# Performance work log

Measured on AMD Instinct MI355X. Metric: run time of the kernel, lower is better.

Reference implementation:

```python
import jax, jax.numpy as jnp
import numpy as np

# TT-factorized linear: 784 = 7*4*7*4 -> 512 = 4*4*8*4, max_rank=20
# canonical TT ranks: [1, 20, 20, 16, 1] (r3 capped by m4*n4 = 16)
B = 16384
R1, R2, R3 = 20, 20, 16


def setup_inputs() -> dict:
    key = jax.random.key(0)
    k = jax.random.split(key, 6)
    x = jax.random.normal(k[0], (B, 784), jnp.float32)
    # TT cores G_k[r_{k-1}, m_k, n_k, r_k] with boundary ranks squeezed
    core1 = jax.random.normal(k[1], (7, 4, R1), jnp.float32) * 0.3   # [m1,n1,r1]
    core2 = jax.random.normal(k[2], (R1, 4, 4, R2), jnp.float32) * 0.1  # [r1,m2,n2,r2]
    core3 = jax.random.normal(k[3], (R2, 7, 8, R3), jnp.float32) * 0.05  # [r2,m3,n3,r3]
    core4 = jax.random.normal(k[4], (R3, 4, 4), jnp.float32) * 0.1   # [r3,m4,n4]
    bias = jax.random.normal(k[5], (512,), jnp.float32) * 0.01
    return {"x": x, "core1": core1, "core2": core2, "core3": core3,
            "core4": core4, "bias": bias}


def reference(x, core1, core2, core3, core4, bias):
    b = x.shape[0]
    # reshape input into TT mode factorization [B, m1, m2, m3, m4]
    x5 = x.reshape(b, 7, 4, 7, 4)
    # chain of small core contractions (the fusion-opportunity op pattern)
    t = jnp.einsum('bijkl,ipr->bjklpr', x5, core1)   # [B,4,7,4, n1,r1]
    t = jnp.einsum('bjklpr,rjqs->bklpqs', t, core2)  # [B,7,4, n1,n2,r2]
    t = jnp.einsum('bklpqs,sket->blpqet', t, core3)  # [B,4, n1,n2,n3,r3]
    y = jnp.einsum('blpqet,tlf->bpqef', t, core4)    # [B, n1,n2,n3,n4]
    y = y.reshape(b, 512) + bias
    # original forward: relu then softmax over features.
    # NOTE: the source calls self.fc2(y) but discards the result, so it is
    # omitted here (no effect on output).
    return jax.nn.softmax(jax.nn.relu(y), axis=1)
```

## Files before the change

### kernel.cpp

```cpp
#include <hip/hip_runtime.h>


typedef __attribute__((ext_vector_type(8))) short short8;
typedef __attribute__((ext_vector_type(4))) float floatx4;

__device__ __forceinline__ unsigned int pack2_bf16(float a, float b) {
    unsigned int ua = __float_as_uint(a);
    unsigned int ub = __float_as_uint(b);
    return ((ub + 0x8000u) & 0xFFFF0000u) | ((ua + 0x8000u) >> 16);
}

__device__ __forceinline__ short f32_to_bf16_rne(float v) {
    unsigned int u = __float_as_uint(v);
    return (short)(((u + 0x7FFFu + ((u >> 16) & 1)) >> 16) & 0xFFFF);
}

__global__ void prep_all(const float* __restrict__ c1, const float* __restrict__ c2,
                         const float* __restrict__ c3, const float* __restrict__ c4,
                         short* __restrict__ wp) {
    const int tid = threadIdx.x;
    const int blk = blockIdx.x;
    if (blk == 224) {
        for (int e = tid; e < 8192; e += 256) {
            int j   = e & 7;
            int lid = (e >> 3) & 15;
            int q2  = (e >> 7) & 1;
            int tn  = e >> 8;
            wp[(((tn * 25 + 24) * 64 + (2 + q2) * 16 + lid) << 3) + j] = 0;
        }
        return;
    }
    __shared__ float t12s[320];
    __shared__ float t123s[7 * 256];
    __shared__ float c4s[256];

    const int ij    = blk >> 3;
    const int strip = blk & 7;
    const int i  = ij >> 2, j2 = ij & 3;
    const int p  = strip >> 1;
    const int qh = strip & 1;

    if (tid < 256) c4s[tid] = c4[tid];
    for (int e = tid; e < 320; e += 256) {
        int s = e % 20, pq = e / 20;
        int pp = pq >> 2, q = pq & 3;
        float acc = 0.f;
        #pragma unroll
        for (int r = 0; r < 20; ++r)
            acc += c1[i * 80 + pp * 20 + r] * c2[r * 320 + j2 * 80 + q * 20 + s];
        t12s[e] = acc;
    }
    __syncthreads();

    for (int e = tid; e < 1792; e += 256) {
        int k3 = e >> 8, li = e & 255;
        int t = li & 15, pql = li >> 4;
        int qloc = pql >> 3, e3 = pql & 7;
        int q = 2 * qh + qloc;
        float acc = 0.f;
        const float* tp = t12s + (p * 4 + q) * 20;
        const float* cp = c3 + k3 * 128 + e3 * 16 + t;
        #pragma unroll
        for (int s = 0; s < 20; ++s) acc += tp[s] * cp[s * 896];
        t123s[e] = acc;
    }
    __syncthreads();

    for (int e = tid; e < 1792; e += 256) {
        int kl = e >> 6, nl = e & 63;
        int k = ij * 28 + kl;
        int n = strip * 64 + nl;
        int k3 = kl >> 2, l = kl & 3;
        int f4 = n & 3, e3 = (n >> 2) & 7;
        int pql = ((n >> 5) & 1) * 8 + e3;
        const float* tp = t123s + k3 * 256 + pql * 16;
        const float* cq = c4s + l * 4 + f4;
        float a = 0.f;
        #pragma unroll
        for (int t = 0; t < 16; ++t) a += tp[t] * cq[t * 16];
        int tk = k >> 5, quad = (k >> 3) & 3, j = k & 7;
        int tn = n >> 4, lid = n & 15;
        wp[(((tn * 25 + tk) * 64 + quad * 16 + lid) << 3) + j] = f32_to_bf16_rne(a);
    }
}

__global__ __launch_bounds__(512, 4) void tt_gemm(const float* __restrict__ x,
                                                  const short* __restrict__ wp,
                                                  const float* __restrict__ bias,
                                                  float* __restrict__ out) {
    __shared__ __align__(16) short s_a[3200 * 8];
    __shared__ float part[8][32];

    const int tid  = threadIdx.x;
    const int w    = tid >> 6;
    const int lane = tid & 63;
    const int quad = lane >> 4;
    const int lid  = lane & 15;
    const int m_base = blockIdx.x * 32;

    const short* wpw = wp + ((size_t)(w * 4) * 25 * 64 + lane) * 8;

    short8 b_f[3][4];
    #pragma unroll
    for (int nt = 0; nt < 4; ++nt) {
        b_f[0][nt] = *(const short8*)(wpw + (size_t)(nt * 25 + 0) * 64 * 8);
        b_f[1][nt] = *(const short8*)(wpw + (size_t)(nt * 25 + 1) * 64 * 8);
    }

    for (int a = tid; a < 3200; a += 512) {
        const int row = ((a >> 6) & 1) * 16 + (a & 15);
        const int kc  = ((a >> 7) * 4 + ((a >> 4) & 3)) * 8;
        floatx4 v0 = {0.f, 0.f, 0.f, 0.f}, v1 = {0.f, 0.f, 0.f, 0.f};
        if (kc < 784) {
            const floatx4* pp = (const floatx4*)(x + (size_t)(m_base + row) * 784 + kc);
            v0 = pp[0]; v1 = pp[1];
        }
        union { short8 s; unsigned int u[4]; } af;
        af.u[0] = pack2_bf16(v0.x, v0.y);
        af.u[1] = pack2_bf16(v0.z, v0.w);
        af.u[2] = pack2_bf16(v1.x, v1.y);
        af.u[3] = pack2_bf16(v1.z, v1.w);
        *(short8*)&s_a[a * 8] = af.s;
    }
    __syncthreads();

    const short* sa = s_a + lane * 8;

    floatx4 acc[2][4];
    #pragma unroll
    for (int mt = 0; mt < 2; ++mt)
        #pragma unroll
        for (int nt = 0; nt < 4; ++nt)
            acc[mt][nt] = floatx4{0.f, 0.f, 0.f, 0.f};

    short8 a_f[2][2];
    a_f[0][0] = *(const short8*)(sa);
    a_f[0][1] = *(const short8*)(sa + 64 * 8);

    #pragma unroll
    for (int tk = 0; tk < 25; ++tk) {
        if (tk + 2 < 25) {
            #pragma unroll
            for (int nt = 0; nt < 4; ++nt)
                b_f[(tk + 2) % 3][nt] = *(const short8*)(wpw + (size_t)(nt * 25 + tk + 2) * 64 * 8);
        }
        if (tk + 1 < 25) {
            const short* sa2 = sa + (size_t)(tk + 1) * 128 * 8;
            a_f[(tk + 1) & 1][0] = *(const short8*)(sa2);
            a_f[(tk + 1) & 1][1] = *(const short8*)(sa2 + 64 * 8);
        }
        #pragma unroll
        for (int nt = 0; nt < 4; ++nt) {
            acc[0][nt] = __builtin_amdgcn_mfma_f32_16x16x32_bf16(a_f[tk & 1][0], b_f[tk % 3][nt], acc[0][nt], 0, 0, 0);
            acc[1][nt] = __builtin_amdgcn_mfma_f32_16x16x32_bf16(a_f[tk & 1][1], b_f[tk % 3][nt], acc[1][nt], 0, 0, 0);
        }
    }

    float bias_v[4];
    #pragma unroll
    for (int nt = 0; nt < 4; ++nt)
        bias_v[nt] = bias[w * 64 + nt * 16 + lid];

    #pragma unroll
    for (int mt = 0; mt < 2; ++mt) {
        #pragma unroll
        for (int reg = 0; reg < 4; ++reg) {
            float s = 0.f;
            #pragma unroll
            for (int nt = 0; nt < 4; ++nt) {
                float v = acc[mt][nt][reg] + bias_v[nt];
                v = fmaxf(v, 0.f);
                float e = __expf(v);
                acc[mt][nt][reg] = e;
                s += e;
            }
            s += __shfl_xor(s, 1, 64);
            s += __shfl_xor(s, 2, 64);
            s += __shfl_xor(s, 4, 64);
            s += __shfl_xor(s, 8, 64);
            if (lid == 0) part[w][mt * 16 + quad * 4 + reg] = s;
        }
    }
    __syncthreads();

    #pragma unroll
    for (int mt = 0; mt < 2; ++mt) {
        #pragma unroll
        for (int reg = 0; reg < 4; ++reg) {
            const int row = mt * 16 + quad * 4 + reg;
            float tot = 0.f;
            #pragma unroll
            for (int ww = 0; ww < 8; ++ww) tot += part[ww][row];
            const float inv = 1.0f / tot;
            #pragma unroll
            for (int nt = 0; nt < 4; ++nt)
                out[(size_t)(m_base + row) * 512 + w * 64 + nt * 16 + lid] = acc[mt][nt][reg] * inv;
        }
    }
}

extern "C" void kernel_launch(void* const* d_in, const int* in_sizes, int n_in,
                              void* d_out, int out_size, void* d_ws, size_t ws_size,
                              hipStream_t stream) {
    const float* x    = (const float*)d_in[0];
    const float* c1   = (const float*)d_in[1];
    const float* c2   = (const float*)d_in[2];
    const float* c3   = (const float*)d_in[3];
    const float* c4   = (const float*)d_in[4];
    const float* bias = (const float*)d_in[5];
    float* out = (float*)d_out;
    short* wpb = (short*)d_ws;

    prep_all<<<225, 256, 0, stream>>>(c1, c2, c3, c4, wpb);
    tt_gemm <<<512, 512, 0, stream>>>(x, wpb, bias, out);
}
```

Before: 125.7 us.

## Double-buffer A tile in LDS across five K-chunks to overlap loads with MFMA

Replaces the single full-K staging of the 32x784 activation tile in LDS with a two-buffer scheme over five K-chunks. Global loads for the next chunk are issued before the MFMA work on the current chunk, and are converted and written to LDS afterwards. B fragments are now loaded directly inside the loop rather than software-prefetched three deep. This shrinks LDS use (possibly raising occupancy) and hides global load latency behind compute, at the cost of extra barriers and less explicit B prefetching.

Result: no change. 126.5 us (+0.7%).

```diff
diff --git a/kernel.cpp b/kernel.cpp
--- a/kernel.cpp
+++ b/kernel.cpp
@@ -88,7 +88,7 @@
                                                   const short* __restrict__ wp,
                                                   const float* __restrict__ bias,
                                                   float* __restrict__ out) {
-    __shared__ __align__(16) short s_a[3200 * 8];
+    __shared__ __align__(16) short s_a[2][640 * 8];
     __shared__ float part[8][32];
 
     const int tid  = threadIdx.x;
@@ -97,34 +97,37 @@
     const int quad = lane >> 4;
     const int lid  = lane & 15;
     const int m_base = blockIdx.x * 32;
+    const bool two = (tid < 128);
 
     const short* wpw = wp + ((size_t)(w * 4) * 25 * 64 + lane) * 8;
 
-    short8 b_f[3][4];
-    #pragma unroll
-    for (int nt = 0; nt < 4; ++nt) {
-        b_f[0][nt] = *(const short8*)(wpw + (size_t)(nt * 25 + 0) * 64 * 8);
-        b_f[1][nt] = *(const short8*)(wpw + (size_t)(nt * 25 + 1) * 64 * 8);
-    }
-
-    for (int a = tid; a < 3200; a += 512) {
-        const int row = ((a >> 6) & 1) * 16 + (a & 15);
-        const int kc  = ((a >> 7) * 4 + ((a >> 4) & 3)) * 8;
-        floatx4 v0 = {0.f, 0.f, 0.f, 0.f}, v1 = {0.f, 0.f, 0.f, 0.f};
+    auto stage_load = [&](int c, int e, floatx4& v0, floatx4& v1) {
+        const int row = ((e >> 6) & 1) * 16 + (e & 15);
+        const int kc  = ((c * 5 + (e >> 7)) * 4 + ((e >> 4) & 3)) * 8;
+        v0 = floatx4{0.f, 0.f, 0.f, 0.f};
+        v1 = floatx4{0.f, 0.f, 0.f, 0.f};
         if (kc < 784) {
-            const floatx4* pp = (const floatx4*)(x + (size_t)(m_base + row) * 784 + kc);
-            v0 = pp[0]; v1 = pp[1];
-        }
+            const floatx4* p = (const floatx4*)(x + (size_t)(m_base + row) * 784 + kc);
+            v0 = p[0]; v1 = p[1];
+        }
+    };
+    auto stage_write = [&](int buf, int e, floatx4 v0, floatx4 v1) {
         union { short8 s; unsigned int u[4]; } af;
         af.u[0] = pack2_bf16(v0.x, v0.y);
         af.u[1] = pack2_bf16(v0.z, v0.w);
         af.u[2] = pack2_bf16(v1.x, v1.y);
         af.u[3] = pack2_bf16(v1.z, v1.w);
-        *(short8*)&s_a[a * 8] = af.s;
-    }
-    __syncthreads();
-
-    const short* sa = s_a + lane * 8;
+        *(short8*)&s_a[buf][e * 8] = af.s;
+    };
+
+    {
+        floatx4 a0, a1, b0, b1;
+        stage_load(0, tid, a0, a1);
+        if (two) stage_load(0, 512 + tid, b0, b1);
+        stage_write(0, tid, a0, a1);
+        if (two) stage_write(0, 512 + tid, b0, b1);
+    }
+    __syncthreads();
 
     floatx4 acc[2][4];
     #pragma unroll
@@ -133,26 +136,32 @@
         for (int nt = 0; nt < 4; ++nt)
             acc[mt][nt] = floatx4{0.f, 0.f, 0.f, 0.f};
 
-    short8 a_f[2][2];
-    a_f[0][0] = *(const short8*)(sa);
-    a_f[0][1] = *(const short8*)(sa + 64 * 8);
-
-    #pragma unroll
-    for (int tk = 0; tk < 25; ++tk) {
-        if (tk + 2 < 25) {
-            #pragma unroll
-            for (int nt = 0; nt < 4; ++nt)
-                b_f[(tk + 2) % 3][nt] = *(const short8*)(wpw + (size_t)(nt * 25 + tk + 2) * 64 * 8);
-        }
-        if (tk + 1 < 25) {
-            const short* sa2 = sa + (size_t)(tk + 1) * 128 * 8;
-            a_f[(tk + 1) & 1][0] = *(const short8*)(sa2);
-            a_f[(tk + 1) & 1][1] = *(const short8*)(sa2 + 64 * 8);
-        }
-        #pragma unroll
-        for (int nt = 0; nt < 4; ++nt) {
-            acc[0][nt] = __builtin_amdgcn_mfma_f32_16x16x32_bf16(a_f[tk & 1][0], b_f[tk % 3][nt], acc[0][nt], 0, 0, 0);
-            acc[1][nt] = __builtin_amdgcn_mfma_f32_16x16x32_bf16(a_f[tk & 1][1], b_f[tk % 3][nt], acc[1][nt], 0, 0, 0);
+    #pragma unroll
+    for (int c = 0; c < 5; ++c) {
+        floatx4 p0, p1, q0, q1;
+        if (c + 1 < 5) {
+            stage_load(c + 1, tid, p0, p1);
+            if (two) stage_load(c + 1, 512 + tid, q0, q1);
+        }
+
+        const short* sab = &s_a[c & 1][lane * 8];
+        #pragma unroll
+        for (int tl = 0; tl < 5; ++tl) {
+            short8 a0 = *(const short8*)(sab + (size_t)(tl * 128) * 8);
+            short8 a1 = *(const short8*)(sab + (size_t)(tl * 128 + 64) * 8);
+            const int tk = c * 5 + tl;
+            #pragma unroll
+            for (int nt = 0; nt < 4; ++nt) {
+                short8 bf = *(const short8*)(wpw + (size_t)(nt * 25 + tk) * 64 * 8);
+                acc[0][nt] = __builtin_amdgcn_mfma_f32_16x16x32_bf16(a0, bf, acc[0][nt], 0, 0, 0);
+                acc[1][nt] = __builtin_amdgcn_mfma_f32_16x16x32_bf16(a1, bf, acc[1][nt], 0, 0, 0);
+            }
+        }
+
+        if (c + 1 < 5) {
+            stage_write((c + 1) & 1, tid, p0, p1);
+            if (two) stage_write((c + 1) & 1, 512 + tid, q0, q1);
+            __syncthreads();
         }
     }
 
```

## Double M-tile per block and overlap second-half X loads with first-half MFMAs

Applied to the files above, without the earlier changes.

Each block now handles 64 rows instead of 32, doubling reuse of each B-fragment load across four M sub-tiles. The K dimension is split into two halves: the first half of X is staged to LDS, and the second half's global loads are issued into registers while the first-half MFMAs run, then converted and stored. This hides part of the X load latency and halves the number of weight reloads, at the cost of more registers, occupancy lowered to 2 blocks, a grid of only 256 blocks, and removal of the previous register prefetch of B.

After: 128.3 us. +2.1%, slower.

```diff
diff --git a/kernel.cpp b/kernel.cpp
--- a/kernel.cpp
+++ b/kernel.cpp
@@ -84,76 +84,103 @@
     }
 }
 
-__global__ __launch_bounds__(512, 4) void tt_gemm(const float* __restrict__ x,
+__global__ __launch_bounds__(512, 2) void tt_gemm(const float* __restrict__ x,
                                                   const short* __restrict__ wp,
                                                   const float* __restrict__ bias,
                                                   float* __restrict__ out) {
-    __shared__ __align__(16) short s_a[3200 * 8];
-    __shared__ float part[8][32];
+    __shared__ __align__(16) short s_a0[13 * 256 * 8];
+    __shared__ __align__(16) short s_a1[12 * 256 * 8];
+    __shared__ float part[8][64];
 
     const int tid  = threadIdx.x;
     const int w    = tid >> 6;
     const int lane = tid & 63;
     const int quad = lane >> 4;
     const int lid  = lane & 15;
-    const int m_base = blockIdx.x * 32;
+    const int m_base = blockIdx.x * 64;
 
     const short* wpw = wp + ((size_t)(w * 4) * 25 * 64 + lane) * 8;
 
-    short8 b_f[3][4];
-    #pragma unroll
-    for (int nt = 0; nt < 4; ++nt) {
-        b_f[0][nt] = *(const short8*)(wpw + (size_t)(nt * 25 + 0) * 64 * 8);
-        b_f[1][nt] = *(const short8*)(wpw + (size_t)(nt * 25 + 1) * 64 * 8);
-    }
-
-    for (int a = tid; a < 3200; a += 512) {
-        const int row = ((a >> 6) & 1) * 16 + (a & 15);
-        const int kc  = ((a >> 7) * 4 + ((a >> 4) & 3)) * 8;
-        floatx4 v0 = {0.f, 0.f, 0.f, 0.f}, v1 = {0.f, 0.f, 0.f, 0.f};
-        if (kc < 784) {
-            const floatx4* pp = (const floatx4*)(x + (size_t)(m_base + row) * 784 + kc);
-            v0 = pp[0]; v1 = pp[1];
-        }
+    auto entry_row = [&](int e) { return m_base + ((e >> 6) & 3) * 16 + (e & 15); };
+    auto entry_kc  = [&](int T, int e) { return (T + (e >> 8)) * 32 + ((e >> 4) & 3) * 8; };
+
+    for (int e = tid; e < 13 * 256; e += 512) {
+        const floatx4* p = (const floatx4*)(x + (size_t)entry_row(e) * 784 + entry_kc(0, e));
+        floatx4 v0 = p[0], v1 = p[1];
         union { short8 s; unsigned int u[4]; } af;
         af.u[0] = pack2_bf16(v0.x, v0.y);
         af.u[1] = pack2_bf16(v0.z, v0.w);
         af.u[2] = pack2_bf16(v1.x, v1.y);
         af.u[3] = pack2_bf16(v1.z, v1.w);
-        *(short8*)&s_a[a * 8] = af.s;
-    }
-    __syncthreads();
-
-    const short* sa = s_a + lane * 8;
-
-    floatx4 acc[2][4];
-    #pragma unroll
-    for (int mt = 0; mt < 2; ++mt)
+        *(short8*)&s_a0[e * 8] = af.s;
+    }
+    __syncthreads();
+
+    floatx4 h0[6], h1[6];
+    #pragma unroll
+    for (int i = 0; i < 6; ++i) {
+        const int e  = tid + i * 512;
+        const int kc = entry_kc(13, e);
+        h0[i] = floatx4{0.f, 0.f, 0.f, 0.f};
+        h1[i] = floatx4{0.f, 0.f, 0.f, 0.f};
+        if (kc < 784) {
+            const floatx4* p = (const floatx4*)(x + (size_t)entry_row(e) * 784 + kc);
+            h0[i] = p[0]; h1[i] = p[1];
+        }
+    }
+
+    floatx4 acc[4][4];
+    #pragma unroll
+    for (int mt = 0; mt < 4; ++mt)
         #pragma unroll
         for (int nt = 0; nt < 4; ++nt)
             acc[mt][nt] = floatx4{0.f, 0.f, 0.f, 0.f};
 
-    short8 a_f[2][2];
-    a_f[0][0] = *(const short8*)(sa);
-    a_f[0][1] = *(const short8*)(sa + 64 * 8);
-
-    #pragma unroll
-    for (int tk = 0; tk < 25; ++tk) {
-        if (tk + 2 < 25) {
-            #pragma unroll
-            for (int nt = 0; nt < 4; ++nt)
-                b_f[(tk + 2) % 3][nt] = *(const short8*)(wpw + (size_t)(nt * 25 + tk + 2) * 64 * 8);
-        }
-        if (tk + 1 < 25) {
-            const short* sa2 = sa + (size_t)(tk + 1) * 128 * 8;
-            a_f[(tk + 1) & 1][0] = *(const short8*)(sa2);
-            a_f[(tk + 1) & 1][1] = *(const short8*)(sa2 + 64 * 8);
-        }
-        #pragma unroll
-        for (int nt = 0; nt < 4; ++nt) {
-            acc[0][nt] = __builtin_amdgcn_mfma_f32_16x16x32_bf16(a_f[tk & 1][0], b_f[tk % 3][nt], acc[0][nt], 0, 0, 0);
-            acc[1][nt] = __builtin_amdgcn_mfma_f32_16x16x32_bf16(a_f[tk & 1][1], b_f[tk % 3][nt], acc[1][nt], 0, 0, 0);
-        }
+    const short* sa0 = s_a0 + lane * 8;
+    const short* sa1 = s_a1 + lane * 8;
+
+    #pragma unroll
+    for (int tl = 0; tl < 13; ++tl) {
+        short8 af[4], bf[4];
+        #pragma unroll
+        for (int mt = 0; mt < 4; ++mt)
+            af[mt] = *(const short8*)(sa0 + (size_t)(tl * 256 + mt * 64) * 8);
+        #pragma unroll
+        for (int nt = 0; nt < 4; ++nt)
+            bf[nt] = *(const short8*)(wpw + (size_t)(nt * 25 + tl) * 64 * 8);
+        #pragma unroll
+        for (int nt = 0; nt < 4; ++nt)
+            #pragma unroll
+            for (int mt = 0; mt < 4; ++mt)
+                acc[mt][nt] = __builtin_amdgcn_mfma_f32_16x16x32_bf16(af[mt], bf[nt], acc[mt][nt], 0, 0, 0);
+    }
+
+    #pragma unroll
+    for (int i = 0; i < 6; ++i) {
+        const int e = tid + i * 512;
+        union { short8 s; unsigned int u[4]; } af;
+        af.u[0] = pack2_bf16(h0[i].x, h0[i].y);
+        af.u[1] = pack2_bf16(h0[i].z, h0[i].w);
+        af.u[2] = pack2_bf16(h1[i].x, h1[i].y);
+        af.u[3] = pack2_bf16(h1[i].z, h1[i].w);
+        *(short8*)&s_a1[e * 8] = af.s;
+    }
+    __syncthreads();
+
+    #pragma unroll
+    for (int tl = 0; tl < 12; ++tl) {
+        short8 af[4], bf[4];
+        #pragma unroll
+        for (int mt = 0; mt < 4; ++mt)
+            af[mt] = *(const short8*)(sa1 + (size_t)(tl * 256 + mt * 64) * 8);
+        #pragma unroll
+        for (int nt = 0; nt < 4; ++nt)
+            bf[nt] = *(const short8*)(wpw + (size_t)(nt * 25 + 13 + tl) * 64 * 8);
+        #pragma unroll
+        for (int nt = 0; nt < 4; ++nt)
+            #pragma unroll
+            for (int mt = 0; mt < 4; ++mt)
+                acc[mt][nt] = __builtin_amdgcn_mfma_f32_16x16x32_bf16(af[mt], bf[nt], acc[mt][nt], 0, 0, 0);
     }
 
     float bias_v[4];
@@ -162,7 +189,7 @@
         bias_v[nt] = bias[w * 64 + nt * 16 + lid];
 
     #pragma unroll
-    for (int mt = 0; mt < 2; ++mt) {
+    for (int mt = 0; mt < 4; ++mt) {
         #pragma unroll
         for (int reg = 0; reg < 4; ++reg) {
             float s = 0.f;
@@ -184,7 +211,7 @@
     __syncthreads();
 
     #pragma unroll
-    for (int mt = 0; mt < 2; ++mt) {
+    for (int mt = 0; mt < 4; ++mt) {
         #pragma unroll
         for (int reg = 0; reg < 4; ++reg) {
             const int row = mt * 16 + quad * 4 + reg;
@@ -212,5 +239,5 @@
     short* wpb = (short*)d_ws;
 
     prep_all<<<225, 256, 0, stream>>>(c1, c2, c3, c4, wpb);
-    tt_gemm <<<512, 512, 0, stream>>>(x, wpb, bias, out);
-}
+    tt_gemm <<<256, 512, 0, stream>>>(x, wpb, bias, out);
+}
```

## Pre-convert x to bf16 fragment layout and stream it via global_load_lds

Applied to the files above, without the earlier changes.

Adds a separate kernel that converts x to bf16 in MFMA fragment order in workspace. The GEMM then double-buffers 64-wide K tiles into LDS with direct global-to-LDS loads instead of staging all of K up front. LDS use drops from about 51KB to 8KB, which should allow more blocks per CU. K is padded to 26 steps to match. The cost is an extra kernel launch plus a full write and re-read of a bf16 copy of x, and per-tile block syncs inside the K loop.

Result: slower. 136.1 us (+8.3%).

```diff
diff --git a/kernel.cpp b/kernel.cpp
--- a/kernel.cpp
+++ b/kernel.cpp
@@ -3,6 +3,11 @@
 
 typedef __attribute__((ext_vector_type(8))) short short8;
 typedef __attribute__((ext_vector_type(4))) float floatx4;
+typedef __attribute__((address_space(1))) const unsigned int gu32;
+typedef __attribute__((address_space(3))) unsigned int lu32;
+
+#define XT_OFF 0
+#define WP_OFF 27262976
 
 __device__ __forceinline__ unsigned int pack2_bf16(float a, float b) {
     unsigned int ua = __float_as_uint(a);
@@ -13,6 +18,28 @@
 __device__ __forceinline__ short f32_to_bf16_rne(float v) {
     unsigned int u = __float_as_uint(v);
     return (short)(((u + 0x7FFFu + ((u >> 16) & 1)) >> 16) & 0xFFFF);
+}
+
+__global__ void conv_x(const float* __restrict__ x, short* __restrict__ xt) {
+    const int g = blockIdx.x * 256 + threadIdx.x;
+    const int c    = g & 255;
+    const int mbkt = g >> 8;
+    const int kt = mbkt % 13;
+    const int mb = mbkt / 13;
+    const int ks = c >> 7, mt = (c >> 6) & 1, quad = (c >> 4) & 3, lid = c & 15;
+    const int row = mb * 32 + mt * 16 + lid;
+    const int k0  = kt * 64 + ks * 32 + quad * 8;
+    floatx4 v0 = {0.f, 0.f, 0.f, 0.f}, v1 = {0.f, 0.f, 0.f, 0.f};
+    if (k0 < 784) {
+        const floatx4* p = (const floatx4*)(x + (size_t)row * 784 + k0);
+        v0 = p[0]; v1 = p[1];
+    }
+    union { short8 s; unsigned int u[4]; } af;
+    af.u[0] = pack2_bf16(v0.x, v0.y);
+    af.u[1] = pack2_bf16(v0.z, v0.w);
+    af.u[2] = pack2_bf16(v1.x, v1.y);
+    af.u[3] = pack2_bf16(v1.z, v1.w);
+    *(short8*)(xt + (size_t)g * 8) = af.s;
 }
 
 __global__ void prep_all(const float* __restrict__ c1, const float* __restrict__ c2,
@@ -21,12 +48,15 @@
     const int tid = threadIdx.x;
     const int blk = blockIdx.x;
     if (blk == 224) {
-        for (int e = tid; e < 8192; e += 256) {
-            int j   = e & 7;
-            int lid = (e >> 3) & 15;
-            int q2  = (e >> 7) & 1;
-            int tn  = e >> 8;
-            wp[(((tn * 25 + 24) * 64 + (2 + q2) * 16 + lid) << 3) + j] = 0;
+        for (int e = tid; e < 24576; e += 256) {
+            int tn = e / 768;
+            int r  = e % 768;
+            int qq = r >> 7;
+            int lid = (r >> 3) & 15;
+            int j  = r & 7;
+            int tks  = (qq < 2) ? 24 : 25;
+            int quad = (qq < 2) ? (2 + qq) : (qq - 2);
+            wp[(((tn * 26 + tks) * 64 + quad * 16 + lid) << 3) + j] = 0;
         }
         return;
     }
@@ -78,17 +108,17 @@
         float a = 0.f;
         #pragma unroll
         for (int t = 0; t < 16; ++t) a += tp[t] * cq[t * 16];
-        int tk = k >> 5, quad = (k >> 3) & 3, j = k & 7;
+        int tks = k >> 5, quad = (k >> 3) & 3, j = k & 7;
         int tn = n >> 4, lid = n & 15;
-        wp[(((tn * 25 + tk) * 64 + quad * 16 + lid) << 3) + j] = f32_to_bf16_rne(a);
-    }
-}
-
-__global__ __launch_bounds__(512, 4) void tt_gemm(const float* __restrict__ x,
+        wp[(((tn * 26 + tks) * 64 + quad * 16 + lid) << 3) + j] = f32_to_bf16_rne(a);
+    }
+}
+
+__global__ __launch_bounds__(512, 4) void tt_gemm(const short* __restrict__ xt,
                                                   const short* __restrict__ wp,
                                                   const float* __restrict__ bias,
                                                   float* __restrict__ out) {
-    __shared__ __align__(16) short s_a[3200 * 8];
+    __shared__ __align__(16) short s_a[2][2048];
     __shared__ float part[8][32];
 
     const int tid  = threadIdx.x;
@@ -96,35 +126,20 @@
     const int lane = tid & 63;
     const int quad = lane >> 4;
     const int lid  = lane & 15;
-    const int m_base = blockIdx.x * 32;
-
-    const short* wpw = wp + ((size_t)(w * 4) * 25 * 64 + lane) * 8;
-
-    short8 b_f[3][4];
-    #pragma unroll
-    for (int nt = 0; nt < 4; ++nt) {
-        b_f[0][nt] = *(const short8*)(wpw + (size_t)(nt * 25 + 0) * 64 * 8);
-        b_f[1][nt] = *(const short8*)(wpw + (size_t)(nt * 25 + 1) * 64 * 8);
-    }
-
-    for (int a = tid; a < 3200; a += 512) {
-        const int row = ((a >> 6) & 1) * 16 + (a & 15);
-        const int kc  = ((a >> 7) * 4 + ((a >> 4) & 3)) * 8;
-        floatx4 v0 = {0.f, 0.f, 0.f, 0.f}, v1 = {0.f, 0.f, 0.f, 0.f};
-        if (kc < 784) {
-            const floatx4* pp = (const floatx4*)(x + (size_t)(m_base + row) * 784 + kc);
-            v0 = pp[0]; v1 = pp[1];
-        }
-        union { short8 s; unsigned int u[4]; } af;
-        af.u[0] = pack2_bf16(v0.x, v0.y);
-        af.u[1] = pack2_bf16(v0.z, v0.w);
-        af.u[2] = pack2_bf16(v1.x, v1.y);
-        af.u[3] = pack2_bf16(v1.z, v1.w);
-        *(short8*)&s_a[a * 8] = af.s;
-    }
-    __syncthreads();
-
-    const short* sa = s_a + lane * 8;
+    const int mb   = blockIdx.x;
+    const int m_base = mb * 32;
+
+    const short* wpw = wp + ((size_t)(w * 4) * 26 * 64 + lane) * 8;
+
+    auto stage = [&](int kt, int buf) {
+        if (w < 4) {
+            const short* g = xt + (size_t)(mb * 13 + kt) * 2048 + w * 512 + lane * 8;
+            __builtin_amdgcn_global_load_lds((gu32*)g, (lu32*)&s_a[buf][w * 512], 16, 0, 0);
+        }
+    };
+
+    stage(0, 0);
+    __syncthreads();
 
     floatx4 acc[2][4];
     #pragma unroll
@@ -133,27 +148,24 @@
         for (int nt = 0; nt < 4; ++nt)
             acc[mt][nt] = floatx4{0.f, 0.f, 0.f, 0.f};
 
-    short8 a_f[2][2];
-    a_f[0][0] = *(const short8*)(sa);
-    a_f[0][1] = *(const short8*)(sa + 64 * 8);
-
-    #pragma unroll
-    for (int tk = 0; tk < 25; ++tk) {
-        if (tk + 2 < 25) {
-            #pragma unroll
-            for (int nt = 0; nt < 4; ++nt)
-                b_f[(tk + 2) % 3][nt] = *(const short8*)(wpw + (size_t)(nt * 25 + tk + 2) * 64 * 8);
-        }
-        if (tk + 1 < 25) {
-            const short* sa2 = sa + (size_t)(tk + 1) * 128 * 8;
-            a_f[(tk + 1) & 1][0] = *(const short8*)(sa2);
-            a_f[(tk + 1) & 1][1] = *(const short8*)(sa2 + 64 * 8);
-        }
-        #pragma unroll
-        for (int nt = 0; nt < 4; ++nt) {
-            acc[0][nt] = __builtin_amdgcn_mfma_f32_16x16x32_bf16(a_f[tk & 1][0], b_f[tk % 3][nt], acc[0][nt], 0, 0, 0);
-            acc[1][nt] = __builtin_amdgcn_mfma_f32_16x16x32_bf16(a_f[tk & 1][1], b_f[tk % 3][nt], acc[1][nt], 0, 0, 0);
-        }
+    #pragma unroll 1
+    for (int kt = 0; kt < 13; ++kt) {
+        if (kt + 1 < 13) stage(kt + 1, (kt + 1) & 1);
+
+        const short* sab = &s_a[kt & 1][lane * 8];
+        #pragma unroll
+        for (int ks = 0; ks < 2; ++ks) {
+            short8 a0 = *(const short8*)(sab + (ks * 128) * 8);
+            short8 a1 = *(const short8*)(sab + (ks * 128 + 64) * 8);
+            const int tks = kt * 2 + ks;
+            #pragma unroll
+            for (int nt = 0; nt < 4; ++nt) {
+                short8 bf = *(const short8*)(wpw + (size_t)(nt * 26 + tks) * 64 * 8);
+                acc[0][nt] = __builtin_amdgcn_mfma_f32_16x16x32_bf16(a0, bf, acc[0][nt], 0, 0, 0);
+                acc[1][nt] = __builtin_amdgcn_mfma_f32_16x16x32_bf16(a1, bf, acc[1][nt], 0, 0, 0);
+            }
+        }
+        __syncthreads();
     }
 
     float bias_v[4];
@@ -209,8 +221,12 @@
     const float* c4   = (const float*)d_in[4];
     const float* bias = (const float*)d_in[5];
     float* out = (float*)d_out;
-    short* wpb = (short*)d_ws;
-
-    prep_all<<<225, 256, 0, stream>>>(c1, c2, c3, c4, wpb);
-    tt_gemm <<<512, 512, 0, stream>>>(x, wpb, bias, out);
-}
+
+    char* ws = (char*)d_ws;
+    short* xt  = (short*)(ws + XT_OFF);
+    short* wpb = (short*)(ws + WP_OFF);
+
+    conv_x  <<<6656, 256, 0, stream>>>(x, xt);
+    prep_all<<<225,  256, 0, stream>>>(c1, c2, c3, c4, wpb);
+    tt_gemm <<<512,  512, 0, stream>>>(xt, wpb, bias, out);
+}
```
